# Optimization experiments

Hardware: AMD Instinct MI355X
Metric: run time of the kernel (lower is better)

## Reference

```python
import jax, jax.numpy as jnp
import numpy as np

LEVEL_N = [81920, 20480, 5120, 1280, 320]  # faces at div..div-4 (div=6, 20*4^d)
K = 10  # SpherePHD conv kernel taps
W_SHAPES = [(64,3),(64,64),(128,64),(128,128),(256,128),(256,256),(256,256),(512,256),(512,512),(512,512),(512,512),(512,512),(512,512)]
BLOCKS = [[0,1],[2,3],[4,5,6],[7,8,9],[10,11,12]]  # conv indices per VGG block


def setup_inputs() -> dict:
    key = jax.random.key(0)
    ks = iter(jax.random.split(key, 64))
    d = {"x": jax.random.normal(next(ks), (2, 3, LEVEL_N[0]), jnp.float32)}
    for l, n in enumerate(LEVEL_N):
        d[f"conv_t{l}"] = jax.random.randint(next(ks), (n, K), 0, n, jnp.int32)
        d[f"adj_t{l}"] = jax.random.randint(next(ks), (n, 4), 0, n, jnp.int32)
        d[f"pool_t{l}"] = jax.random.randint(next(ks), (n // 4,), 0, n, jnp.int32)
    for i, (o, c) in enumerate(W_SHAPES):
        d[f"w{i}"] = jax.random.normal(next(ks), (o, c, K), jnp.float32) * (1.0 / np.sqrt(c * K))
        d[f"b{i}"] = jnp.zeros((o,), jnp.float32)
    return d


def phd_conv(x, w, b, table):
    # x: [B,C,N], table: [N,K] -> gather neighbors [B,C,N,K], weighted sum, ReLU
    g = x[:, :, table]
    y = jnp.einsum('bcnk,ock->bon', g, w) + b[None, :, None]
    return jax.nn.relu(y)


def phd_maxpool(x, adj, pool):
    # max over adjacent faces, then subsample to parent faces
    m = jnp.max(x[:, :, adj], axis=-1)  # [B,C,N]
    return m[:, :, pool]                # [B,C,N/4]


def reference(x, conv_t0, conv_t1, conv_t2, conv_t3, conv_t4,
              adj_t0, adj_t1, adj_t2, adj_t3, adj_t4,
              pool_t0, pool_t1, pool_t2, pool_t3, pool_t4,
              w0, w1, w2, w3, w4, w5, w6, w7, w8, w9, w10, w11, w12,
              b0, b1, b2, b3, b4, b5, b6, b7, b8, b9, b10, b11, b12):
    conv_ts = [conv_t0, conv_t1, conv_t2, conv_t3, conv_t4]
    adj_ts = [adj_t0, adj_t1, adj_t2, adj_t3, adj_t4]
    pool_ts = [pool_t0, pool_t1, pool_t2, pool_t3, pool_t4]
    ws = [w0, w1, w2, w3, w4, w5, w6, w7, w8, w9, w10, w11, w12]
    bs = [b0, b1, b2, b3, b4, b5, b6, b7, b8, b9, b10, b11, b12]
    h = x
    for lvl, idxs in enumerate(BLOCKS):
        for i in idxs:
            h = phd_conv(h, ws[i], bs[i], conv_ts[lvl])
        h = phd_maxpool(h, adj_ts[lvl], pool_ts[lvl])
    return h  # [2, 512, 80]
```

## Files before the change

kernel.cpp:

```cpp
#include <hip/hip_runtime.h>
#include <stdint.h>

typedef __bf16 bf16;
typedef bf16 bf16x8 __attribute__((ext_vector_type(8)));
typedef float f32x4 __attribute__((ext_vector_type(4)));
typedef unsigned short u16x8 __attribute__((ext_vector_type(8)));

__device__ __forceinline__ void gload_lds16(const bf16* g, bf16* l) {
    __builtin_amdgcn_global_load_lds(
        (const __attribute__((address_space(1))) void*)g,
        (__attribute__((address_space(3))) void*)l, 16, 0, 0);
}

template<int C>
__device__ inline void cvt_one(const float* __restrict__ src, bf16* __restrict__ dst,
                               int e, int base) {
    int local = e - base;
    constexpr int CK = C * 10;
    int o = local / CK;
    int rem = local - o * CK;
    int k = rem / C;
    int c = rem & (C - 1);
    dst[e] = (bf16)src[(o * C + c) * 10 + k];
}

__global__ __launch_bounds__(256) void prep_w(
    const float* w1, const float* w2, const float* w3, const float* w4,
    const float* w5, const float* w6, const float* w7, const float* w8,
    const float* w9, const float* w10, const float* w11, const float* w12,
    bf16* __restrict__ dst)
{
    int e = blockIdx.x * 256 + threadIdx.x;
    if (e >= 16343040) return;
    if      (e <    40960) cvt_one< 64>(w1,  dst, e, 0);
    else if (e <   122880) cvt_one< 64>(w2,  dst, e, 40960);
    else if (e <   286720) cvt_one<128>(w3,  dst, e, 122880);
    else if (e <   614400) cvt_one<128>(w4,  dst, e, 286720);
    else if (e <  1269760) cvt_one<256>(w5,  dst, e, 614400);
    else if (e <  1925120) cvt_one<256>(w6,  dst, e, 1269760);
    else if (e <  3235840) cvt_one<256>(w7,  dst, e, 1925120);
    else if (e <  5857280) cvt_one<512>(w8,  dst, e, 3235840);
    else if (e <  8478720) cvt_one<512>(w9,  dst, e, 5857280);
    else if (e < 11100160) cvt_one<512>(w10, dst, e, 8478720);
    else if (e < 13721600) cvt_one<512>(w11, dst, e, 11100160);
    else                   cvt_one<512>(w12, dst, e, 13721600);
}

__global__ __launch_bounds__(256) void conv0_kernel(
    const float* __restrict__ x, const float* __restrict__ w0,
    const float* __restrict__ b0, const int* __restrict__ table,
    bf16* __restrict__ out)
{
    const int N = 81920;
    __shared__ float wls[30][64];
    __shared__ float bls[64];
    int tid = threadIdx.x;
    for (int i = tid; i < 1920; i += 256) {
        int o = i / 30, ck = i - o * 30;
        wls[ck][o] = w0[i];
    }
    if (tid < 64) bls[tid] = b0[tid];
    __syncthreads();

    int p = blockIdx.x * 256 + tid;
    int b = p >= N;
    int n = p - b * N;
    int idx[10];
    const int* trow = table + n * 10;
#pragma unroll
    for (int k = 0; k < 10; k++) idx[k] = trow[k];
    float xv[30];
#pragma unroll
    for (int c = 0; c < 3; c++)
#pragma unroll
        for (int k = 0; k < 10; k++)
            xv[c * 10 + k] = x[(b * 3 + c) * N + idx[k]];

    float acc[64];
#pragma unroll
    for (int o = 0; o < 64; o++) acc[o] = bls[o];
    for (int ck = 0; ck < 30; ck++) {
        float xs = xv[ck];
        const f32x4* wrow = (const f32x4*)(&wls[ck][0]);
#pragma unroll
        for (int o4 = 0; o4 < 16; o4++) {
            f32x4 w4 = wrow[o4];
            acc[o4 * 4 + 0] += xs * w4[0];
            acc[o4 * 4 + 1] += xs * w4[1];
            acc[o4 * 4 + 2] += xs * w4[2];
            acc[o4 * 4 + 3] += xs * w4[3];
        }
    }
    bf16x8 ob[8];
#pragma unroll
    for (int i = 0; i < 8; i++)
#pragma unroll
        for (int e = 0; e < 8; e++)
            ob[i][e] = (bf16)fmaxf(acc[i * 8 + e], 0.0f);
    bf16x8* dst = (bf16x8*)(out + (size_t)p * 64);
#pragma unroll
    for (int i = 0; i < 8; i++) dst[i] = ob[i];
}

template<int C>
__global__ __launch_bounds__(256) void conv_p(
    const bf16* __restrict__ in, const bf16* __restrict__ w,
    const float* __restrict__ bias, const int* __restrict__ table,
    bf16* __restrict__ out, float* __restrict__ slab,
    int N, int O, int S, int PO)
{
    constexpr int CH = C / 64;
    constexpr int CHUNKS = CH * 10;
    constexpr int CK = C * 10;
    __shared__ bf16 Xs[3][64][64];
    __shared__ bf16 Ws[3][64][64];
    __shared__ int rowoff[64][10];

    const int tid = threadIdx.x;
    const int lane = tid & 63;
    const int wid = tid >> 6;
    const int wo = wid & 1, wp = wid >> 1;
    const int l16 = lane & 15, q = lane >> 4;

    const int p0 = blockIdx.x * 64;
    const int o0 = blockIdx.y * 64;
    const int z = blockIdx.z;

    for (int j = tid; j < 640; j += 256) {
        int pp = j / 10, k = j - pp * 10;
        int p = p0 + pp;
        int b = p >= N;
        int n = p - b * N;
        rowoff[pp][k] = (b * N + table[n * 10 + k]) * C;
    }
    __syncthreads();

    int srowv[2], gsegv[2];
    const bf16* wbase[2];
#pragma unroll
    for (int t = 0; t < 2; t++) {
        int row = wid * 16 + t * 8 + (lane >> 3);
        int gs = (lane & 7) ^ (row & 7);
        srowv[t] = row; gsegv[t] = gs;
        wbase[t] = w + (size_t)(o0 + row) * CK + gs * 8;
    }

    const int per = CHUNKS / S;
    const int c0chunk = z * per;

    auto stage = [&](int chunk, int b3) {
        int k = chunk / CH;
        int cofs = (chunk & (CH - 1)) * 64;
#pragma unroll
        for (int t = 0; t < 2; t++) {
            int ro = rowoff[srowv[t]][k];
            gload_lds16(in + ro + cofs + gsegv[t] * 8, &Xs[b3][wid * 16 + t * 8][0]);
            gload_lds16(wbase[t] + chunk * 64, &Ws[b3][wid * 16 + t * 8][0]);
        }
    };

    f32x4 acc[2][2];
#pragma unroll
    for (int a = 0; a < 2; a++)
#pragma unroll
        for (int c = 0; c < 2; c++) acc[a][c] = (f32x4){0.f, 0.f, 0.f, 0.f};

    stage(c0chunk, 0);
    stage(c0chunk + 1, 1);

    const int arow = wo * 32 + l16;
    const int brow = wp * 32 + l16;
    const int sx = l16 & 7;

    int bi = 0, bs = 2;
    for (int i = 0; i < per; i++) {
        asm volatile("s_waitcnt vmcnt(4)" ::: "memory");
        __builtin_amdgcn_s_barrier();
        const bf16* xb = &Xs[bi][0][0];
        const bf16* wb = &Ws[bi][0][0];
#pragma unroll
        for (int ks = 0; ks < 2; ks++) {
            int slot = ((ks * 4 + q) ^ sx) * 8;
            bf16x8 af[2], bfr[2];
#pragma unroll
            for (int to = 0; to < 2; to++)
                af[to] = *(const bf16x8*)(wb + (arow + to * 16) * 64 + slot);
#pragma unroll
            for (int tp = 0; tp < 2; tp++)
                bfr[tp] = *(const bf16x8*)(xb + (brow + tp * 16) * 64 + slot);
#pragma unroll
            for (int to = 0; to < 2; to++)
#pragma unroll
                for (int tp = 0; tp < 2; tp++)
                    acc[to][tp] = __builtin_amdgcn_mfma_f32_16x16x32_bf16(
                        af[to], bfr[tp], acc[to][tp], 0, 0, 0);
        }
        int nx = i + 2 < per ? i + 2 : per - 1;
        stage(c0chunk + nx, bs);
        bi = bi == 2 ? 0 : bi + 1;
        bs = bs == 2 ? 0 : bs + 1;
    }

    if (S == 1) {
#pragma unroll
        for (int to = 0; to < 2; ++to) {
            int ob = o0 + wo * 32 + to * 16 + q * 4;
            f32x4 bv = *(const f32x4*)(bias + ob);
#pragma unroll
            for (int tp = 0; tp < 2; ++tp) {
                int p = p0 + wp * 32 + tp * 16 + l16;
                union { ushort4 u4; unsigned short s[4]; } pk;
#pragma unroll
                for (int r = 0; r < 4; r++) {
                    float v = fmaxf(acc[to][tp][r] + bv[r], 0.0f);
                    union { bf16 h; unsigned short u; } cc;
                    cc.h = (bf16)v;
                    pk.s[r] = cc.u;
                }
                *(ushort4*)(out + (size_t)p * O + ob) = pk.u4;
            }
        }
    } else {
        float* sb = slab + (size_t)z * PO;
#pragma unroll
        for (int to = 0; to < 2; ++to) {
            int ob = o0 + wo * 32 + to * 16 + q * 4;
#pragma unroll
            for (int tp = 0; tp < 2; ++tp) {
                int p = p0 + wp * 32 + tp * 16 + l16;
                *(f32x4*)(sb + (size_t)p * O + ob) = acc[to][tp];
            }
        }
    }
}

__global__ __launch_bounds__(256) void epi_reduce(
    const float* __restrict__ slab, const float* __restrict__ bias,
    bf16* __restrict__ out, int PO, int Omask, int S)
{
    int t4 = (blockIdx.x * 256 + threadIdx.x) * 4;
    if (t4 >= PO) return;
    f32x4 s = *(const f32x4*)(slab + t4);
    for (int zz = 1; zz < S; zz++)
        s += *(const f32x4*)(slab + (size_t)zz * PO + t4);
    int o = t4 & Omask;
    f32x4 bv = *(const f32x4*)(bias + o);
    union { ushort4 u4; unsigned short e[4]; } pk;
#pragma unroll
    for (int r = 0; r < 4; r++) {
        float v = fmaxf(s[r] + bv[r], 0.0f);
        union { bf16 h; unsigned short u; } cc;
        cc.h = (bf16)v;
        pk.e[r] = cc.u;
    }
    *(ushort4*)((unsigned short*)out + t4) = pk.u4;
}

__global__ __launch_bounds__(256) void pool_kernel(
    const bf16* __restrict__ in, const int* __restrict__ adj,
    const int* __restrict__ pool, bf16* __restrict__ out,
    int N, int M, int c8shift)
{
    int t = blockIdx.x * 256 + threadIdx.x;
    int total = M << c8shift;
    if (t >= total) return;
    int cc = t & ((1 << c8shift) - 1);
    int j = t >> c8shift;
    int b = blockIdx.y;
    int C = 8 << c8shift;
    int s = pool[j];
    const int* a = adj + s * 4;
    const unsigned short* inu = (const unsigned short*)in;
    size_t base = (size_t)b * N * C + (size_t)cc * 8;
    u16x8 m = *(const u16x8*)(inu + base + (size_t)a[0] * C);
#pragma unroll
    for (int i = 1; i < 4; i++) {
        u16x8 v = *(const u16x8*)(inu + base + (size_t)a[i] * C);
#pragma unroll
        for (int e = 0; e < 8; e++) m[e] = v[e] > m[e] ? v[e] : m[e];
    }
    *(u16x8*)((unsigned short*)out + ((size_t)b * M + j) * C + (size_t)cc * 8) = m;
}

__global__ __launch_bounds__(256) void final_pool(
    const bf16* __restrict__ in, const int* __restrict__ adj,
    const int* __restrict__ pool, float* __restrict__ out)
{
    int t = blockIdx.x * 256 + threadIdx.x;
    if (t >= 81920) return;
    int j = t % 80;
    int rest = t / 80;
    int c = rest & 511;
    int b = rest >> 9;
    int s = pool[j];
    const int* a = adj + s * 4;
    float m = 0.0f;
#pragma unroll
    for (int i = 0; i < 4; i++) {
        float v = (float)in[((size_t)b * 320 + a[i]) * 512 + c];
        m = fmaxf(m, v);
    }
    out[t] = m;
}

extern "C" void kernel_launch(void* const* d_in, const int* in_sizes, int n_in,
                              void* d_out, int out_size, void* d_ws, size_t ws_size,
                              hipStream_t stream)
{
    const float* x = (const float*)d_in[0];
    const int* convT[5]; const int* adjT[5]; const int* poolT[5];
    for (int l = 0; l < 5; l++) {
        convT[l] = (const int*)d_in[1 + 3 * l];
        adjT[l]  = (const int*)d_in[2 + 3 * l];
        poolT[l] = (const int*)d_in[3 + 3 * l];
    }
    const float* W[13]; const float* Bs[13];
    for (int i = 0; i < 13; i++) {
        W[i]  = (const float*)d_in[16 + 2 * i];
        Bs[i] = (const float*)d_in[17 + 2 * i];
    }

    bf16* wbf = (bf16*)d_ws;
    bf16* A  = (bf16*)((char*)d_ws + (size_t)16343040 * 2);
    bf16* Bb = A + 10485760;
    float* slabA = (float*)((char*)A + (6u << 20));
    float* slabB = (float*)((char*)Bb + (6u << 20));

    static const int woff[13] = {0, 0, 40960, 122880, 286720, 614400, 1269760,
                                 1925120, 3235840, 5857280, 8478720, 11100160, 13721600};

    prep_w<<<dim3((16343040 + 255) / 256), dim3(256), 0, stream>>>(
        W[1], W[2], W[3], W[4], W[5], W[6], W[7], W[8], W[9], W[10], W[11], W[12], wbf);

    conv0_kernel<<<dim3(640), dim3(256), 0, stream>>>(x, W[0], Bs[0], convT[0], A);

    const int PO3 = 2560 * 512;
    const int PO4 = 640 * 512;

    conv_p<64><<<dim3(2560, 1, 1), dim3(256), 0, stream>>>(A, wbf + woff[1], Bs[1], convT[0], Bb, nullptr, 81920, 64, 1, 0);
    pool_kernel<<<dim3(640, 2), dim3(256), 0, stream>>>(Bb, adjT[0], poolT[0], A, 81920, 20480, 3);
    conv_p<64><<<dim3(640, 2, 1), dim3(256), 0, stream>>>(A, wbf + woff[2], Bs[2], convT[1], Bb, nullptr, 20480, 128, 1, 0);
    conv_p<128><<<dim3(640, 2, 1), dim3(256), 0, stream>>>(Bb, wbf + woff[3], Bs[3], convT[1], A, nullptr, 20480, 128, 1, 0);
    pool_kernel<<<dim3(320, 2), dim3(256), 0, stream>>>(A, adjT[1], poolT[1], Bb, 20480, 5120, 4);
    conv_p<128><<<dim3(160, 4, 1), dim3(256), 0, stream>>>(Bb, wbf + woff[4], Bs[4], convT[2], A, nullptr, 5120, 256, 1, 0);
    conv_p<256><<<dim3(160, 4, 1), dim3(256), 0, stream>>>(A, wbf + woff[5], Bs[5], convT[2], Bb, nullptr, 5120, 256, 1, 0);
    conv_p<256><<<dim3(160, 4, 1), dim3(256), 0, stream>>>(Bb, wbf + woff[6], Bs[6], convT[2], A, nullptr, 5120, 256, 1, 0);
    pool_kernel<<<dim3(160, 2), dim3(256), 0, stream>>>(A, adjT[2], poolT[2], Bb, 5120, 1280, 5);
    conv_p<256><<<dim3(40, 8, 2), dim3(256), 0, stream>>>(Bb, wbf + woff[7], Bs[7], convT[3], nullptr, slabA, 1280, 512, 2, PO3);
    epi_reduce<<<dim3(PO3 / 1024), dim3(256), 0, stream>>>(slabA, Bs[7], A, PO3, 511, 2);
    conv_p<512><<<dim3(40, 8, 2), dim3(256), 0, stream>>>(A, wbf + woff[8], Bs[8], convT[3], nullptr, slabB, 1280, 512, 2, PO3);
    epi_reduce<<<dim3(PO3 / 1024), dim3(256), 0, stream>>>(slabB, Bs[8], Bb, PO3, 511, 2);
    conv_p<512><<<dim3(40, 8, 2), dim3(256), 0, stream>>>(Bb, wbf + woff[9], Bs[9], convT[3], nullptr, slabA, 1280, 512, 2, PO3);
    epi_reduce<<<dim3(PO3 / 1024), dim3(256), 0, stream>>>(slabA, Bs[9], A, PO3, 511, 2);
    pool_kernel<<<dim3(80, 2), dim3(256), 0, stream>>>(A, adjT[3], poolT[3], Bb, 1280, 320, 6);
    conv_p<512><<<dim3(10, 8, 8), dim3(256), 0, stream>>>(Bb, wbf + woff[10], Bs[10], convT[4], nullptr, slabA, 320, 512, 8, PO4);
    epi_reduce<<<dim3(PO4 / 1024), dim3(256), 0, stream>>>(slabA, Bs[10], A, PO4, 511, 8);
    conv_p<512><<<dim3(10, 8, 8), dim3(256), 0, stream>>>(A, wbf + woff[11], Bs[11], convT[4], nullptr, slabB, 320, 512, 8, PO4);
    epi_reduce<<<dim3(PO4 / 1024), dim3(256), 0, stream>>>(slabB, Bs[11], Bb, PO4, 511, 8);
    conv_p<512><<<dim3(10, 8, 8), dim3(256), 0, stream>>>(Bb, wbf + woff[12], Bs[12], convT[4], nullptr, slabA, 320, 512, 8, PO4);
    epi_reduce<<<dim3(PO4 / 1024), dim3(256), 0, stream>>>(slabA, Bs[12], A, PO4, 511, 8);

    final_pool<<<dim3(320), dim3(256), 0, stream>>>(A, adjT[4], poolT[4], (float*)d_out);
}
```

Before: 556.1 us.

## Pre-swizzle weights into MFMA fragment layout and load directly from global

Replaces the weight transpose kernel with one that writes bf16 weights already arranged in per-lane MFMA A-fragment order. The conv kernel then reads weight fragments straight from global memory instead of staging them through LDS. It also templatizes the output and pixel tile sizes, using larger tiles, and re-balances the split-K factors with a single shared slab. The change cuts LDS traffic and barrier pressure for weights, at the cost of uncached-looking global reads per MFMA step and more reduction passes for the deeper levels.

New measurement: 658.0 us. 18.3% more time.

```diff
diff --git a/kernel.cpp b/kernel.cpp
--- a/kernel.cpp
+++ b/kernel.cpp
@@ -12,38 +12,59 @@
         (__attribute__((address_space(3))) void*)l, 16, 0, 0);
 }
 
-template<int C>
-__device__ inline void cvt_one(const float* __restrict__ src, bf16* __restrict__ dst,
-                               int e, int base) {
-    int local = e - base;
-    constexpr int CK = C * 10;
-    int o = local / CK;
-    int rem = local - o * CK;
-    int k = rem / C;
-    int c = rem & (C - 1);
-    dst[e] = (bf16)src[(o * C + c) * 10 + k];
-}
-
-__global__ __launch_bounds__(256) void prep_w(
-    const float* w1, const float* w2, const float* w3, const float* w4,
-    const float* w5, const float* w6, const float* w7, const float* w8,
-    const float* w9, const float* w10, const float* w11, const float* w12,
-    bf16* __restrict__ dst)
-{
-    int e = blockIdx.x * 256 + threadIdx.x;
-    if (e >= 16343040) return;
-    if      (e <    40960) cvt_one< 64>(w1,  dst, e, 0);
-    else if (e <   122880) cvt_one< 64>(w2,  dst, e, 40960);
-    else if (e <   286720) cvt_one<128>(w3,  dst, e, 122880);
-    else if (e <   614400) cvt_one<128>(w4,  dst, e, 286720);
-    else if (e <  1269760) cvt_one<256>(w5,  dst, e, 614400);
-    else if (e <  1925120) cvt_one<256>(w6,  dst, e, 1269760);
-    else if (e <  3235840) cvt_one<256>(w7,  dst, e, 1925120);
-    else if (e <  5857280) cvt_one<512>(w8,  dst, e, 3235840);
-    else if (e <  8478720) cvt_one<512>(w9,  dst, e, 5857280);
-    else if (e < 11100160) cvt_one<512>(w10, dst, e, 8478720);
-    else if (e < 13721600) cvt_one<512>(w11, dst, e, 11100160);
-    else                   cvt_one<512>(w12, dst, e, 13721600);
+struct PrepArgs {
+    const float* src[12];
+    int base[12];
+    int dstoff[12];
+    int Clog[12];
+    int OT[12];
+    int nClog[12];
+};
+
+__global__ __launch_bounds__(256) void prep_frag(PrepArgs a, bf16* __restrict__ dst)
+{
+    __shared__ bf16 lds[16 * 648];
+    int bid = blockIdx.x;
+    int l = 0;
+#pragma unroll
+    for (int i = 1; i < 12; i++) if (bid >= a.base[i]) l = i;
+    int local = bid - a.base[l];
+    int nClog = a.nClog[l];
+    int cchunk = local & ((1 << nClog) - 1);
+    int ot = local >> nClog;
+    int Clog = a.Clog[l];
+    int CK10 = 10 << Clog;
+    const float* src = a.src[l];
+    int t = threadIdx.x;
+
+    size_t sbase = (size_t)(ot * 16) * CK10 + (size_t)cchunk * 640;
+#pragma unroll
+    for (int it = 0; it < 10; it++) {
+        int idx = t + it * 256;
+        int m = idx / 160;
+        int i4 = idx - m * 160;
+        float4 v = *(const float4*)(src + sbase + (size_t)m * CK10 + i4 * 4);
+        bf16 b4[4] = {(bf16)v.x, (bf16)v.y, (bf16)v.z, (bf16)v.w};
+        *(ushort4*)(&lds[m * 648 + i4 * 4]) = *(ushort4*)b4;
+    }
+    __syncthreads();
+
+    int sub = t >> 6, ll = t & 63;
+    int m = ll & 15, q = ll >> 4;
+    int OTl = a.OT[l];
+    size_t dbase = (size_t)a.dstoff[l];
+#pragma unroll
+    for (int tt = 0; tt < 5; tt++) {
+        int tile = sub + tt * 4;
+        int k = tile >> 1, half = tile & 1;
+        int k32 = (k << (Clog - 5)) + cchunk * 2 + half;
+        bf16 tmp[8];
+#pragma unroll
+        for (int j = 0; j < 8; j++)
+            tmp[j] = lds[m * 648 + (half * 32 + q * 8 + j) * 10 + k];
+        *(bf16x8*)(dst + dbase + ((size_t)(k32 * OTl + ot) << 9) + ll * 8) =
+            *(bf16x8*)tmp;
+    }
 }
 
 __global__ __launch_bounds__(256) void conv0_kernel(
@@ -102,19 +123,18 @@
     for (int i = 0; i < 8; i++) dst[i] = ob[i];
 }
 
-template<int C>
-__global__ __launch_bounds__(256) void conv_p(
-    const bf16* __restrict__ in, const bf16* __restrict__ w,
+template<int C, int TO, int TP>
+__global__ __launch_bounds__(256) void conv_f(
+    const bf16* __restrict__ in, const bf16* __restrict__ wfrag,
     const float* __restrict__ bias, const int* __restrict__ table,
     bf16* __restrict__ out, float* __restrict__ slab,
     int N, int O, int S, int PO)
 {
+    constexpr int BP = TP * 32;
     constexpr int CH = C / 64;
     constexpr int CHUNKS = CH * 10;
-    constexpr int CK = C * 10;
-    __shared__ bf16 Xs[3][64][64];
-    __shared__ bf16 Ws[3][64][64];
-    __shared__ int rowoff[64][10];
+    __shared__ bf16 Xs[3][BP][64];
+    __shared__ int rowoff[BP][10];
 
     const int tid = threadIdx.x;
     const int lane = tid & 63;
@@ -122,11 +142,13 @@
     const int wo = wid & 1, wp = wid >> 1;
     const int l16 = lane & 15, q = lane >> 4;
 
-    const int p0 = blockIdx.x * 64;
-    const int o0 = blockIdx.y * 64;
+    const int p0 = blockIdx.x * BP;
+    const int o0 = blockIdx.y * (TO * 32);
     const int z = blockIdx.z;
-
-    for (int j = tid; j < 640; j += 256) {
+    const int OT = O >> 4;
+    const int stride32 = OT * 512;
+
+    for (int j = tid; j < BP * 10; j += 256) {
         int pp = j / 10, k = j - pp * 10;
         int p = p0 + pp;
         int b = p >= N;
@@ -135,41 +157,39 @@
     }
     __syncthreads();
 
-    int srowv[2], gsegv[2];
-    const bf16* wbase[2];
-#pragma unroll
-    for (int t = 0; t < 2; t++) {
-        int row = wid * 16 + t * 8 + (lane >> 3);
-        int gs = (lane & 7) ^ (row & 7);
-        srowv[t] = row; gsegv[t] = gs;
-        wbase[t] = w + (size_t)(o0 + row) * CK + gs * 8;
-    }
+    const int lrow = lane >> 3;
+    const int gs = (lane & 7) ^ lrow;
+    int srow[TP];
+#pragma unroll
+    for (int t = 0; t < TP; t++) srow[t] = wid * (TP * 8) + t * 8 + lrow;
+
+    const bf16* wfp[TO];
+#pragma unroll
+    for (int to = 0; to < TO; to++)
+        wfp[to] = wfrag + (size_t)((o0 >> 4) + wo * TO + to) * 512 + lane * 8;
 
     const int per = CHUNKS / S;
-    const int c0chunk = z * per;
+    const int ck0 = z * per;
 
     auto stage = [&](int chunk, int b3) {
         int k = chunk / CH;
         int cofs = (chunk & (CH - 1)) * 64;
 #pragma unroll
-        for (int t = 0; t < 2; t++) {
-            int ro = rowoff[srowv[t]][k];
-            gload_lds16(in + ro + cofs + gsegv[t] * 8, &Xs[b3][wid * 16 + t * 8][0]);
-            gload_lds16(wbase[t] + chunk * 64, &Ws[b3][wid * 16 + t * 8][0]);
-        }
+        for (int t = 0; t < TP; t++)
+            gload_lds16(in + rowoff[srow[t]][k] + cofs + gs * 8,
+                        &Xs[b3][wid * (TP * 8) + t * 8][0]);
     };
 
-    f32x4 acc[2][2];
-#pragma unroll
-    for (int a = 0; a < 2; a++)
-#pragma unroll
-        for (int c = 0; c < 2; c++) acc[a][c] = (f32x4){0.f, 0.f, 0.f, 0.f};
-
-    stage(c0chunk, 0);
-    stage(c0chunk + 1, 1);
-
-    const int arow = wo * 32 + l16;
-    const int brow = wp * 32 + l16;
+    f32x4 acc[TO][TP];
+#pragma unroll
+    for (int a = 0; a < TO; a++)
+#pragma unroll
+        for (int c = 0; c < TP; c++) acc[a][c] = (f32x4){0.f, 0.f, 0.f, 0.f};
+
+    stage(ck0, 0);
+    stage(ck0 + 1, 1);
+
+    const int browb = wp * (TP * 16);
     const int sx = l16 & 7;
 
     int bi = 0, bs = 2;
@@ -177,38 +197,39 @@
         asm volatile("s_waitcnt vmcnt(4)" ::: "memory");
         __builtin_amdgcn_s_barrier();
         const bf16* xb = &Xs[bi][0][0];
-        const bf16* wb = &Ws[bi][0][0];
+        const int kt = ck0 + i;
 #pragma unroll
         for (int ks = 0; ks < 2; ks++) {
+            size_t wofs = (size_t)(kt * 2 + ks) * stride32;
             int slot = ((ks * 4 + q) ^ sx) * 8;
-            bf16x8 af[2], bfr[2];
-#pragma unroll
-            for (int to = 0; to < 2; to++)
-                af[to] = *(const bf16x8*)(wb + (arow + to * 16) * 64 + slot);
-#pragma unroll
-            for (int tp = 0; tp < 2; tp++)
-                bfr[tp] = *(const bf16x8*)(xb + (brow + tp * 16) * 64 + slot);
-#pragma unroll
-            for (int to = 0; to < 2; to++)
-#pragma unroll
-                for (int tp = 0; tp < 2; tp++)
+            bf16x8 af[TO], bfr[TP];
+#pragma unroll
+            for (int to = 0; to < TO; to++)
+                af[to] = *(const bf16x8*)(wfp[to] + wofs);
+#pragma unroll
+            for (int tp = 0; tp < TP; tp++)
+                bfr[tp] = *(const bf16x8*)(xb + (browb + tp * 16 + l16) * 64 + slot);
+#pragma unroll
+            for (int to = 0; to < TO; to++)
+#pragma unroll
+                for (int tp = 0; tp < TP; tp++)
                     acc[to][tp] = __builtin_amdgcn_mfma_f32_16x16x32_bf16(
                         af[to], bfr[tp], acc[to][tp], 0, 0, 0);
         }
         int nx = i + 2 < per ? i + 2 : per - 1;
-        stage(c0chunk + nx, bs);
+        stage(ck0 + nx, bs);
         bi = bi == 2 ? 0 : bi + 1;
         bs = bs == 2 ? 0 : bs + 1;
     }
 
     if (S == 1) {
 #pragma unroll
-        for (int to = 0; to < 2; ++to) {
-            int ob = o0 + wo * 32 + to * 16 + q * 4;
+        for (int to = 0; to < TO; ++to) {
+            int ob = o0 + wo * (TO * 16) + to * 16 + q * 4;
             f32x4 bv = *(const f32x4*)(bias + ob);
 #pragma unroll
-            for (int tp = 0; tp < 2; ++tp) {
-                int p = p0 + wp * 32 + tp * 16 + l16;
+            for (int tp = 0; tp < TP; ++tp) {
+                int p = p0 + browb + tp * 16 + l16;
                 union { ushort4 u4; unsigned short s[4]; } pk;
 #pragma unroll
                 for (int r = 0; r < 4; r++) {
@@ -223,11 +244,11 @@
     } else {
         float* sb = slab + (size_t)z * PO;
 #pragma unroll
-        for (int to = 0; to < 2; ++to) {
-            int ob = o0 + wo * 32 + to * 16 + q * 4;
-#pragma unroll
-            for (int tp = 0; tp < 2; ++tp) {
-                int p = p0 + wp * 32 + tp * 16 + l16;
+        for (int to = 0; to < TO; ++to) {
+            int ob = o0 + wo * (TO * 16) + to * 16 + q * 4;
+#pragma unroll
+            for (int tp = 0; tp < TP; ++tp) {
+                int p = p0 + browb + tp * 16 + l16;
                 *(f32x4*)(sb + (size_t)p * O + ob) = acc[to][tp];
             }
         }
@@ -323,42 +344,59 @@
     bf16* wbf = (bf16*)d_ws;
     bf16* A  = (bf16*)((char*)d_ws + (size_t)16343040 * 2);
     bf16* Bb = A + 10485760;
-    float* slabA = (float*)((char*)A + (6u << 20));
-    float* slabB = (float*)((char*)Bb + (6u << 20));
+    float* slab = (float*)((char*)(Bb + 10485760));
 
     static const int woff[13] = {0, 0, 40960, 122880, 286720, 614400, 1269760,
                                  1925120, 3235840, 5857280, 8478720, 11100160, 13721600};
 
-    prep_w<<<dim3((16343040 + 255) / 256), dim3(256), 0, stream>>>(
-        W[1], W[2], W[3], W[4], W[5], W[6], W[7], W[8], W[9], W[10], W[11], W[12], wbf);
+    PrepArgs pa;
+    {
+        static const int clog[12]  = {6,6,7,7,8,8,8,9,9,9,9,9};
+        static const int otl[12]   = {4,8,8,16,16,16,32,32,32,32,32,32};
+        static const int nclog[12] = {0,0,1,1,2,2,2,3,3,3,3,3};
+        static const int basev[12] = {0,4,12,28,60,124,188,316,572,828,1084,1340};
+        for (int i = 0; i < 12; i++) {
+            pa.src[i] = W[i + 1];
+            pa.base[i] = basev[i];
+            pa.dstoff[i] = woff[i + 1];
+            pa.Clog[i] = clog[i];
+            pa.OT[i] = otl[i];
+            pa.nClog[i] = nclog[i];
+        }
+    }
+    prep_frag<<<dim3(1596), dim3(256), 0, stream>>>(pa, wbf);
 
     conv0_kernel<<<dim3(640), dim3(256), 0, stream>>>(x, W[0], Bs[0], convT[0], A);
 
+    const int PO2 = 10240 * 256;
     const int PO3 = 2560 * 512;
     const int PO4 = 640 * 512;
 
-    conv_p<64><<<dim3(2560, 1, 1), dim3(256), 0, stream>>>(A, wbf + woff[1], Bs[1], convT[0], Bb, nullptr, 81920, 64, 1, 0);
+    conv_f<64,2,4><<<dim3(1280, 1, 1), dim3(256), 0, stream>>>(A, wbf + woff[1], Bs[1], convT[0], Bb, slab, 81920, 64, 1, 0);
     pool_kernel<<<dim3(640, 2), dim3(256), 0, stream>>>(Bb, adjT[0], poolT[0], A, 81920, 20480, 3);
-    conv_p<64><<<dim3(640, 2, 1), dim3(256), 0, stream>>>(A, wbf + woff[2], Bs[2], convT[1], Bb, nullptr, 20480, 128, 1, 0);
-    conv_p<128><<<dim3(640, 2, 1), dim3(256), 0, stream>>>(Bb, wbf + woff[3], Bs[3], convT[1], A, nullptr, 20480, 128, 1, 0);
+    conv_f<64,4,4><<<dim3(320, 1, 1), dim3(256), 0, stream>>>(A, wbf + woff[2], Bs[2], convT[1], Bb, slab, 20480, 128, 1, 0);
+    conv_f<128,4,4><<<dim3(320, 1, 1), dim3(256), 0, stream>>>(Bb, wbf + woff[3], Bs[3], convT[1], A, slab, 20480, 128, 1, 0);
     pool_kernel<<<dim3(320, 2), dim3(256), 0, stream>>>(A, adjT[1], poolT[1], Bb, 20480, 5120, 4);
-    conv_p<128><<<dim3(160, 4, 1), dim3(256), 0, stream>>>(Bb, wbf + woff[4], Bs[4], convT[2], A, nullptr, 5120, 256, 1, 0);
-    conv_p<256><<<dim3(160, 4, 1), dim3(256), 0, stream>>>(A, wbf + woff[5], Bs[5], convT[2], Bb, nullptr, 5120, 256, 1, 0);
-    conv_p<256><<<dim3(160, 4, 1), dim3(256), 0, stream>>>(Bb, wbf + woff[6], Bs[6], convT[2], A, nullptr, 5120, 256, 1, 0);
+    conv_f<128,4,4><<<dim3(80, 2, 2), dim3(256), 0, stream>>>(Bb, wbf + woff[4], Bs[4], convT[2], A, slab, 5120, 256, 2, PO2);
+    epi_reduce<<<dim3(PO2 / 1024), dim3(256), 0, stream>>>(slab, Bs[4], A, PO2, 255, 2);
+    conv_f<256,4,4><<<dim3(80, 2, 2), dim3(256), 0, stream>>>(A, wbf + woff[5], Bs[5], convT[2], Bb, slab, 5120, 256, 2, PO2);
+    epi_reduce<<<dim3(PO2 / 1024), dim3(256), 0, stream>>>(slab, Bs[5], Bb, PO2, 255, 2);
+    conv_f<256,4,4><<<dim3(80, 2, 2), dim3(256), 0, stream>>>(Bb, wbf + woff[6], Bs[6], convT[2], A, slab, 5120, 256, 2, PO2);
+    epi_reduce<<<dim3(PO2 / 1024), dim3(256), 0, stream>>>(slab, Bs[6], A, PO2, 255, 2);
     pool_kernel<<<dim3(160, 2), dim3(256), 0, stream>>>(A, adjT[2], poolT[2], Bb, 5120, 1280, 5);
-    conv_p<256><<<dim3(40, 8, 2), dim3(256), 0, stream>>>(Bb, wbf + woff[7], Bs[7], convT[3], nullptr, slabA, 1280, 512, 2, PO3);
-    epi_reduce<<<dim3(PO3 / 1024), dim3(256), 0, stream>>>(slabA, Bs[7], A, PO3, 511, 2);
-    conv_p<512><<<dim3(40, 8, 2), dim3(256), 0, stream>>>(A, wbf + woff[8], Bs[8], convT[3], nullptr, slabB, 1280, 512, 2, PO3);
-    epi_reduce<<<dim3(PO3 / 1024), dim3(256), 0, stream>>>(slabB, Bs[8], Bb, PO3, 511, 2);
-    conv_p<512><<<dim3(40, 8, 2), dim3(256), 0, stream>>>(Bb, wbf + woff[9], Bs[9], convT[3], nullptr, slabA, 1280, 512, 2, PO3);
-    epi_reduce<<<dim3(PO3 / 1024), dim3(256), 0, stream>>>(slabA, Bs[9], A, PO3, 511, 2);
+    conv_f<256,4,4><<<dim3(20, 4, 4), dim3(256), 0, stream>>>(Bb, wbf + woff[7], Bs[7], convT[3], A, slab, 1280, 512, 4, PO3);
+    epi_reduce<<<dim3(PO3 / 1024), dim3(256), 0, stream>>>(slab, Bs[7], A, PO3, 511, 4);
+    conv_f<512,4,4><<<dim3(20, 4, 4), dim3(256), 0, stream>>>(A, wbf + woff[8], Bs[8], convT[3], Bb, slab, 1280, 512, 4, PO3);
+    epi_reduce<<<dim3(PO3 / 1024), dim3(256), 0, stream>>>(slab, Bs[8], Bb, PO3, 511, 4);
+    conv_f<512,4,4><<<dim3(20, 4, 4), dim3(256), 0, stream>>>(Bb, wbf + woff[9], Bs[9], convT[3], A, slab, 1280, 512, 4, PO3);
+    epi_reduce<<<dim3(PO3 / 1024), dim3(256), 0, stream>>>(slab, Bs[9], A, PO3, 511, 4);
     pool_kernel<<<dim3(80, 2), dim3(256), 0, stream>>>(A, adjT[3], poolT[3], Bb, 1280, 320, 6);
-    conv_p<512><<<dim3(10, 8, 8), dim3(256), 0, stream>>>(Bb, wbf + woff[10], Bs[10], convT[4], nullptr, slabA, 320, 512, 8, PO4);
-    epi_reduce<<<dim3(PO4 / 1024), dim3(256), 0, stream>>>(slabA, Bs[10], A, PO4, 511, 8);
-    conv_p<512><<<dim3(10, 8, 8), dim3(256), 0, stream>>>(A, wbf + woff[11], Bs[11], convT[4], nullptr, slabB, 320, 512, 8, PO4);
-    epi_reduce<<<dim3(PO4 / 1024), dim3(256), 0, stream>>>(slabB, Bs[11], Bb, PO4, 511, 8);
-    conv_p<512><<<dim3(10, 8, 8), dim3(256), 0, stream>>>(Bb, wbf + woff[12], Bs[12], convT[4], nullptr, slabA, 320, 512, 8, PO4);
-    epi_reduce<<<dim3(PO4 / 1024), dim3(256), 0, stream>>>(slabA, Bs[12], A, PO4, 511, 8);
+    conv_f<512,4,4><<<dim3(5, 4, 16), dim3(256), 0, stream>>>(Bb, wbf + woff[10], Bs[10], convT[4], A, slab, 320, 512, 16, PO4);
+    epi_reduce<<<dim3(PO4 / 1024), dim3(256), 0, stream>>>(slab, Bs[10], A, PO4, 511, 16);
+    conv_f<512,4,4><<<dim3(5, 4, 16), dim3(256), 0, stream>>>(A, wbf + woff[11], Bs[11], convT[4], Bb, slab, 320, 512, 16, PO4);
+    epi_reduce<<<dim3(PO4 / 1024), dim3(256), 0, stream>>>(slab, Bs[11], Bb, PO4, 511, 16);
+    conv_f<512,4,4><<<dim3(5, 4, 16), dim3(256), 0, stream>>>(Bb, wbf + woff[12], Bs[12], convT[4], A, slab, 320, 512, 16, PO4);
+    epi_reduce<<<dim3(PO4 / 1024), dim3(256), 0, stream>>>(slab, Bs[12], A, PO4, 511, 16);
 
     final_pool<<<dim3(320), dim3(256), 0, stream>>>(A, adjT[4], poolT[4], (float*)d_out);
 }
```
